# Kernel tuning notes

Hardware: AMD Instinct MI355X
Metric: run time of the kernel (lower is better)

## Reference

```python
import jax, jax.numpy as jnp
import numpy as np
from jax import lax

NT = 100
NUM_LEVELS = 9

_KERNEL = jnp.array([[0.0, 0.25, 0.0],
                     [0.25, 0.0, 0.25],
                     [0.0, 0.25, 0.0]], dtype=jnp.float32).reshape(1, 1, 3, 3)


def _conv(x):
    # 3x3 Jacobi stencil, padding=1 (SAME), NCHW layout
    return lax.conv_general_dilated(x, _KERNEL.astype(x.dtype), (1, 1), 'SAME',
                                    dimension_numbers=('NCHW', 'OIHW', 'NCHW'))


def _avg_pool2(x):
    n, c, h, w = x.shape
    return x.reshape(n, c, h // 2, 2, w // 2, 2).mean(axis=(3, 5))


def _interp(x, th, tw):
    n, c = x.shape[:2]
    # bilinear, align_corners=False (half-pixel centers) == jax.image bilinear
    return jax.image.resize(x, (n, c, th, tw), method='bilinear')


def _jacobi(x, mask, nt):
    def step(x, _):
        x_next = _conv(x)
        return x_next * mask + x * (1 - mask), None
    x, _ = lax.scan(step, x, None, length=nt)
    return x


def setup_inputs() -> dict:
    key = jax.random.key(0)
    ks = jax.random.split(key, 12)
    inp = {'X': jax.random.normal(ks[0], (1, 1, 1024, 1024), dtype=jnp.float32)}
    sizes = [1024, 512, 256, 128, 64, 32, 16, 8, 4, 4]
    for i, s in enumerate(sizes):
        inp[f'Mask{i + 1}'] = jax.random.uniform(ks[i + 1], (1, 1, s, s), dtype=jnp.float32)
    return inp


def reference(X, Mask1, Mask2, Mask3, Mask4, Mask5, Mask6, Mask7, Mask8, Mask9, Mask10):
    masks = [Mask1, Mask2, Mask3, Mask4, Mask5, Mask6, Mask7, Mask8, Mask9, Mask10]
    grids = [X]
    # Restriction sweep: fine -> coarse
    for level in range(1, NUM_LEVELS):
        g = grids[level - 1]
        m = masks[level - 1]
        masked_out = _conv(g * (m > 0).astype(g.dtype))
        unmasked_out = _conv(g * (1 - m))
        residual = masked_out + unmasked_out
        grids.append(_avg_pool2(residual))
    # Coarse solve: Jacobi relaxation on coarsest grid with Mask9
    grids[-1] = _jacobi(grids[-1], Mask9, NT)
    # Prolongation sweep: coarse -> fine
    for level in range(NUM_LEVELS - 2, -1, -1):
        th, tw = grids[level].shape[-2:]
        fine = _interp(grids[level + 1], th, tw) + grids[level]
        m = masks[level]
        fine = _conv(fine * (m > 0).astype(fine.dtype)) + _conv(fine * (1 - m))
        grids[level + 1] = fine  # mirror torch list mutation semantics loosely
    # torch code pops down to grids[0] (original X) and runs fine Jacobi on it
    final_solution = grids[0]
    final_solution = _jacobi(final_solution, Mask1, NT)
    return final_solution
```

## Files before the change

### kernel.cpp

```cpp
#include <hip/hip_runtime.h>


#define W 1024
#define H 1024
#define TILE_W 128
#define TILE_H 64
#define TI 10
#define OS_X 104
#define OS_Y 44
#define HX 12
#define NBX 10
#define NBY 24
#define NLAUNCH 10

#define SRr 18
#define SRc 34
#define S_T 0
#define S_B 1
#define S_L 2
#define S_R 3

__device__ __forceinline__ float4 ld4(const float* __restrict__ p, int gr, int gc) {
    if ((unsigned)gr < (unsigned)H && (unsigned)gc < (unsigned)W)
        return *(const float4*)&p[gr * W + gc];
    return make_float4(0.f, 0.f, 0.f, 0.f);
}

__device__ __forceinline__ float4 rowstep(const float4 up, const float4 ce,
                                          const float4 dn, const float lf,
                                          const float rt, const float4 m) {
    float4 s, n;
    s.x = (up.x + dn.x) + (lf   + ce.y);
    s.y = (up.y + dn.y) + (ce.x + ce.z);
    s.z = (up.z + dn.z) + (ce.y + ce.w);
    s.w = (up.w + dn.w) + (ce.z + rt);
    n.x = fmaf(m.x, fmaf(0.25f, s.x, -ce.x), ce.x);
    n.y = fmaf(m.y, fmaf(0.25f, s.y, -ce.y), ce.y);
    n.z = fmaf(m.z, fmaf(0.25f, s.z, -ce.z), ce.z);
    n.w = fmaf(m.w, fmaf(0.25f, s.w, -ce.w), ce.w);
    return n;
}

__global__ __launch_bounds__(512, 1) void jacobi_trap(
    const float* __restrict__ xin, const float* __restrict__ mask,
    float* __restrict__ xout)
{
    __shared__ float4 S[2][4][SRr][SRc];

    const int tid = threadIdx.x;
    const int pr = tid >> 5;
    const int pc = tid & 31;
    const int gx0 = (int)blockIdx.x * OS_X - HX;
    const int gy0 = (int)blockIdx.y * OS_Y - TI;
    const int gr0 = gy0 + pr * 4;
    const int gc0 = gx0 + pc * 4;

    {
        float4* flat = &S[0][0][0][0];
        const int tot = 2 * 4 * SRr * SRc;
        #pragma unroll
        for (int k = 0; k < 10; ++k) {
            int idx = tid + k * 512;
            if (idx < tot) flat[idx] = make_float4(0.f, 0.f, 0.f, 0.f);
        }
    }

    float4 c[4], m[4];
    #pragma unroll
    for (int i = 0; i < 4; ++i) {
        c[i] = ld4(xin,  gr0 + i, gc0);
        m[i] = ld4(mask, gr0 + i, gc0);
    }

    __syncthreads();

    S[0][S_T][pr + 1][pc + 1] = c[0];
    S[0][S_B][pr + 1][pc + 1] = c[3];
    S[0][S_L][pr + 1][pc + 1] = make_float4(c[0].x, c[1].x, c[2].x, c[3].x);
    S[0][S_R][pr + 1][pc + 1] = make_float4(c[0].w, c[1].w, c[2].w, c[3].w);
    __syncthreads();

    #pragma unroll 1
    for (int it = 0; it < TI; ++it) {
        const int rb = it & 1;
        const float4 th = S[rb][S_B][pr    ][pc + 1];
        const float4 bh = S[rb][S_T][pr + 2][pc + 1];
        const float4 lh = S[rb][S_R][pr + 1][pc    ];
        const float4 rh = S[rb][S_L][pr + 1][pc + 2];

        const float4 n0 = rowstep(th,   c[0], c[1], lh.x, rh.x, m[0]);
        const float4 n1 = rowstep(c[0], c[1], c[2], lh.y, rh.y, m[1]);
        const float4 n2 = rowstep(c[1], c[2], c[3], lh.z, rh.z, m[2]);
        const float4 n3 = rowstep(c[2], c[3], bh,   lh.w, rh.w, m[3]);
        c[0] = n0; c[1] = n1; c[2] = n2; c[3] = n3;

        if (it < TI - 1) {
            const int wb = rb ^ 1;
            S[wb][S_T][pr + 1][pc + 1] = n0;
            S[wb][S_B][pr + 1][pc + 1] = n3;
            S[wb][S_L][pr + 1][pc + 1] = make_float4(n0.x, n1.x, n2.x, n3.x);
            S[wb][S_R][pr + 1][pc + 1] = make_float4(n0.w, n1.w, n2.w, n3.w);
            __syncthreads();
        }
    }

    const int lc = pc * 4;
    if (lc >= HX && lc < HX + OS_X && (unsigned)gc0 < (unsigned)W) {
        #pragma unroll
        for (int i = 0; i < 4; ++i) {
            int lr = pr * 4 + i;
            if (lr < TI || lr >= TILE_H - TI) continue;
            int gr = gy0 + lr;
            if ((unsigned)gr >= (unsigned)H) continue;
            *(float4*)&xout[gr * W + gc0] = c[i];
        }
    }
}

extern "C" void kernel_launch(void* const* d_in, const int* in_sizes, int n_in,
                              void* d_out, int out_size, void* d_ws, size_t ws_size,
                              hipStream_t stream) {
    const float* X = (const float*)d_in[0];
    const float* M = (const float*)d_in[1];
    float* out = (float*)d_out;
    float* ws  = (float*)d_ws;

    dim3 grid(NBX, NBY), block(512);
    const float* src = X;
    for (int l = 0; l < NLAUNCH; ++l) {
        float* dst = (l & 1) ? out : ws;
        jacobi_trap<<<grid, block, 0, stream>>>(src, M, dst);
        src = dst;
    }
}
```

Before: 114.6 us.

## Fuse 20 Jacobi steps per launch with 128x128 tiles and 8-row thread strips

Each thread now holds 8 rows instead of 4, so a block covers a 128x128 tile. The kernel runs 20 time steps per launch with a 20-cell halo, cutting the number of launches from 10 to 5. Only the shared-memory border cells are zeroed rather than the whole buffer. The trade is more redundant halo work (88x88 useful output per 128x128 tile), higher register pressure, and fewer blocks (144) to fill the GPU.

Result: slower. 141.7 us (+23.6%).

```diff
diff --git a/kernel.cpp b/kernel.cpp
--- a/kernel.cpp
+++ b/kernel.cpp
@@ -3,22 +3,20 @@
 
 #define W 1024
 #define H 1024
-#define TILE_W 128
-#define TILE_H 64
-#define TI 10
-#define OS_X 104
-#define OS_Y 44
-#define HX 12
-#define NBX 10
-#define NBY 24
-#define NLAUNCH 10
+#define TILE 128
+#define TI 20
+#define OS 88
+#define NB 12
+#define NLAUNCH 5
 
 #define SRr 18
 #define SRc 34
-#define S_T 0
-#define S_B 1
-#define S_L 2
-#define S_R 3
+#define S_T  0
+#define S_B  1
+#define S_L0 2
+#define S_L1 3
+#define S_R0 4
+#define S_R1 5
 
 __device__ __forceinline__ float4 ld4(const float* __restrict__ p, int gr, int gc) {
     if ((unsigned)gr < (unsigned)H && (unsigned)gc < (unsigned)W)
@@ -45,71 +43,86 @@
     const float* __restrict__ xin, const float* __restrict__ mask,
     float* __restrict__ xout)
 {
-    __shared__ float4 S[2][4][SRr][SRc];
+    __shared__ float4 S[2][6][SRr][SRc];
 
     const int tid = threadIdx.x;
     const int pr = tid >> 5;
     const int pc = tid & 31;
-    const int gx0 = (int)blockIdx.x * OS_X - HX;
-    const int gy0 = (int)blockIdx.y * OS_Y - TI;
-    const int gr0 = gy0 + pr * 4;
+    const int gx0 = (int)blockIdx.x * OS - TI;
+    const int gy0 = (int)blockIdx.y * OS - TI;
+    const int gr0 = gy0 + pr * 8;
     const int gc0 = gx0 + pc * 4;
 
-    {
-        float4* flat = &S[0][0][0][0];
-        const int tot = 2 * 4 * SRr * SRc;
-        #pragma unroll
-        for (int k = 0; k < 10; ++k) {
-            int idx = tid + k * 512;
-            if (idx < tot) flat[idx] = make_float4(0.f, 0.f, 0.f, 0.f);
+    #pragma unroll
+    for (int k = 0; k < 3; ++k) {
+        int idx = tid + k * 512;
+        if (idx < 1200) {
+            int bs  = idx / 100;
+            int pos = idx - bs * 100;
+            float4* st = &S[bs / 6][bs % 6][0][0];
+            int r, cc;
+            if      (pos < 34) { r = 0;            cc = pos;      }
+            else if (pos < 68) { r = SRr - 1;      cc = pos - 34; }
+            else if (pos < 84) { r = pos - 68 + 1; cc = 0;        }
+            else               { r = pos - 84 + 1; cc = SRc - 1;  }
+            st[r * SRc + cc] = make_float4(0.f, 0.f, 0.f, 0.f);
         }
     }
 
-    float4 c[4], m[4];
+    float4 c[8], m[8];
     #pragma unroll
-    for (int i = 0; i < 4; ++i) {
+    for (int i = 0; i < 8; ++i) {
         c[i] = ld4(xin,  gr0 + i, gc0);
         m[i] = ld4(mask, gr0 + i, gc0);
     }
 
-    __syncthreads();
-
-    S[0][S_T][pr + 1][pc + 1] = c[0];
-    S[0][S_B][pr + 1][pc + 1] = c[3];
-    S[0][S_L][pr + 1][pc + 1] = make_float4(c[0].x, c[1].x, c[2].x, c[3].x);
-    S[0][S_R][pr + 1][pc + 1] = make_float4(c[0].w, c[1].w, c[2].w, c[3].w);
+    S[0][S_T ][pr + 1][pc + 1] = c[0];
+    S[0][S_B ][pr + 1][pc + 1] = c[7];
+    S[0][S_L0][pr + 1][pc + 1] = make_float4(c[0].x, c[1].x, c[2].x, c[3].x);
+    S[0][S_L1][pr + 1][pc + 1] = make_float4(c[4].x, c[5].x, c[6].x, c[7].x);
+    S[0][S_R0][pr + 1][pc + 1] = make_float4(c[0].w, c[1].w, c[2].w, c[3].w);
+    S[0][S_R1][pr + 1][pc + 1] = make_float4(c[4].w, c[5].w, c[6].w, c[7].w);
     __syncthreads();
 
     #pragma unroll 1
     for (int it = 0; it < TI; ++it) {
         const int rb = it & 1;
-        const float4 th = S[rb][S_B][pr    ][pc + 1];
-        const float4 bh = S[rb][S_T][pr + 2][pc + 1];
-        const float4 lh = S[rb][S_R][pr + 1][pc    ];
-        const float4 rh = S[rb][S_L][pr + 1][pc + 2];
+        const float4 th  = S[rb][S_B ][pr    ][pc + 1];
+        const float4 bh  = S[rb][S_T ][pr + 2][pc + 1];
+        const float4 lh0 = S[rb][S_R0][pr + 1][pc    ];
+        const float4 lh1 = S[rb][S_R1][pr + 1][pc    ];
+        const float4 rh0 = S[rb][S_L0][pr + 1][pc + 2];
+        const float4 rh1 = S[rb][S_L1][pr + 1][pc + 2];
 
-        const float4 n0 = rowstep(th,   c[0], c[1], lh.x, rh.x, m[0]);
-        const float4 n1 = rowstep(c[0], c[1], c[2], lh.y, rh.y, m[1]);
-        const float4 n2 = rowstep(c[1], c[2], c[3], lh.z, rh.z, m[2]);
-        const float4 n3 = rowstep(c[2], c[3], bh,   lh.w, rh.w, m[3]);
-        c[0] = n0; c[1] = n1; c[2] = n2; c[3] = n3;
+        float4 n[8];
+        n[0] = rowstep(th,   c[0], c[1], lh0.x, rh0.x, m[0]);
+        n[1] = rowstep(c[0], c[1], c[2], lh0.y, rh0.y, m[1]);
+        n[2] = rowstep(c[1], c[2], c[3], lh0.z, rh0.z, m[2]);
+        n[3] = rowstep(c[2], c[3], c[4], lh0.w, rh0.w, m[3]);
+        n[4] = rowstep(c[3], c[4], c[5], lh1.x, rh1.x, m[4]);
+        n[5] = rowstep(c[4], c[5], c[6], lh1.y, rh1.y, m[5]);
+        n[6] = rowstep(c[5], c[6], c[7], lh1.z, rh1.z, m[6]);
+        n[7] = rowstep(c[6], c[7], bh,   lh1.w, rh1.w, m[7]);
+        #pragma unroll
+        for (int i = 0; i < 8; ++i) c[i] = n[i];
 
         if (it < TI - 1) {
             const int wb = rb ^ 1;
-            S[wb][S_T][pr + 1][pc + 1] = n0;
-            S[wb][S_B][pr + 1][pc + 1] = n3;
-            S[wb][S_L][pr + 1][pc + 1] = make_float4(n0.x, n1.x, n2.x, n3.x);
-            S[wb][S_R][pr + 1][pc + 1] = make_float4(n0.w, n1.w, n2.w, n3.w);
+            S[wb][S_T ][pr + 1][pc + 1] = n[0];
+            S[wb][S_B ][pr + 1][pc + 1] = n[7];
+            S[wb][S_L0][pr + 1][pc + 1] = make_float4(n[0].x, n[1].x, n[2].x, n[3].x);
+            S[wb][S_L1][pr + 1][pc + 1] = make_float4(n[4].x, n[5].x, n[6].x, n[7].x);
+            S[wb][S_R0][pr + 1][pc + 1] = make_float4(n[0].w, n[1].w, n[2].w, n[3].w);
+            S[wb][S_R1][pr + 1][pc + 1] = make_float4(n[4].w, n[5].w, n[6].w, n[7].w);
             __syncthreads();
         }
     }
 
-    const int lc = pc * 4;
-    if (lc >= HX && lc < HX + OS_X && (unsigned)gc0 < (unsigned)W) {
+    if (pc >= 5 && pc <= 26 && (unsigned)gc0 < (unsigned)W) {
         #pragma unroll
-        for (int i = 0; i < 4; ++i) {
-            int lr = pr * 4 + i;
-            if (lr < TI || lr >= TILE_H - TI) continue;
+        for (int i = 0; i < 8; ++i) {
+            int lr = pr * 8 + i;
+            if (lr < TI || lr >= TILE - TI) continue;
             int gr = gy0 + lr;
             if ((unsigned)gr >= (unsigned)H) continue;
             *(float4*)&xout[gr * W + gc0] = c[i];
@@ -125,10 +138,10 @@
     float* out = (float*)d_out;
     float* ws  = (float*)d_ws;
 
-    dim3 grid(NBX, NBY), block(512);
+    dim3 grid(NB, NB), block(512);
     const float* src = X;
     for (int l = 0; l < NLAUNCH; ++l) {
-        float* dst = (l & 1) ? out : ws;
+        float* dst = ((NLAUNCH - 1 - l) & 1) ? ws : out;
         jacobi_trap<<<grid, block, 0, stream>>>(src, M, dst);
         src = dst;
     }
```

## Exchange vertical halos within wavefront via permlane32 swap, shrink LDS halo buffers

Applied to the files above, without the earlier changes.

Each 64-lane wavefront holds two tile rows. The halo exchange between those two rows now goes through permlane32_swap in registers instead of LDS. Only the cross-wavefront top and bottom halos still use LDS, in separate smaller arrays, and only their boundary cells are zeroed instead of clearing the whole shared buffer. This removes about half of the top/bottom LDS writes and reads plus the full shared-memory clear. In exchange it adds cross-lane swap instructions and divergent selects between the two half-waves.

After: 102.8 us. 1.11x faster.

```diff
diff --git a/kernel.cpp b/kernel.cpp
--- a/kernel.cpp
+++ b/kernel.cpp
@@ -13,12 +13,7 @@
 #define NBY 24
 #define NLAUNCH 10
 
-#define SRr 18
-#define SRc 34
-#define S_T 0
-#define S_B 1
-#define S_L 2
-#define S_R 3
+typedef unsigned uint2v __attribute__((ext_vector_type(2)));
 
 __device__ __forceinline__ float4 ld4(const float* __restrict__ p, int gr, int gc) {
     if ((unsigned)gr < (unsigned)H && (unsigned)gc < (unsigned)W)
@@ -41,29 +36,39 @@
     return n;
 }
 
+__device__ __forceinline__ float xchg32(float p) {
+    unsigned u = __float_as_uint(p);
+    uint2v r = __builtin_amdgcn_permlane32_swap(u, u, false, false);
+    return __uint_as_float(r.x ^ r.y ^ u);
+}
+
+__device__ __forceinline__ float4 xchg32_4(const float4 p) {
+    return make_float4(xchg32(p.x), xchg32(p.y), xchg32(p.z), xchg32(p.w));
+}
+
+__device__ __forceinline__ float4 sel4(bool c, const float4 a, const float4 b) {
+    return make_float4(c ? a.x : b.x, c ? a.y : b.y,
+                       c ? a.z : b.z, c ? a.w : b.w);
+}
+
 __global__ __launch_bounds__(512, 1) void jacobi_trap(
     const float* __restrict__ xin, const float* __restrict__ mask,
     float* __restrict__ xout)
 {
-    __shared__ float4 S[2][4][SRr][SRc];
+    __shared__ float4 SLs[2][18][34];
+    __shared__ float4 SRs[2][18][34];
+    __shared__ float4 STs[2][10][32];
+    __shared__ float4 SBs[2][10][32];
 
     const int tid = threadIdx.x;
-    const int pr = tid >> 5;
-    const int pc = tid & 31;
+    const int pr  = tid >> 5;
+    const int pc  = tid & 31;
+    const int wid = tid >> 6;
+    const bool lowHalf = (tid & 32) == 0;
     const int gx0 = (int)blockIdx.x * OS_X - HX;
     const int gy0 = (int)blockIdx.y * OS_Y - TI;
     const int gr0 = gy0 + pr * 4;
     const int gc0 = gx0 + pc * 4;
-
-    {
-        float4* flat = &S[0][0][0][0];
-        const int tot = 2 * 4 * SRr * SRc;
-        #pragma unroll
-        for (int k = 0; k < 10; ++k) {
-            int idx = tid + k * 512;
-            if (idx < tot) flat[idx] = make_float4(0.f, 0.f, 0.f, 0.f);
-        }
-    }
 
     float4 c[4], m[4];
     #pragma unroll
@@ -72,21 +77,38 @@
         m[i] = ld4(mask, gr0 + i, gc0);
     }
 
-    __syncthreads();
+    const float4 z4 = make_float4(0.f, 0.f, 0.f, 0.f);
+    if (tid < 72) {
+        int b = tid / 36, r2 = tid % 36;
+        if (r2 < 18) SRs[b][r2][0] = z4;
+        else         SLs[b][r2 - 18][33] = z4;
+    } else if (tid >= 128 && tid < 256) {
+        int j = tid - 128, b = j >> 6, r3 = j & 63;
+        if (r3 < 32) STs[b][9][r3] = z4;
+        else         SBs[b][0][r3 - 32] = z4;
+    }
 
-    S[0][S_T][pr + 1][pc + 1] = c[0];
-    S[0][S_B][pr + 1][pc + 1] = c[3];
-    S[0][S_L][pr + 1][pc + 1] = make_float4(c[0].x, c[1].x, c[2].x, c[3].x);
-    S[0][S_R][pr + 1][pc + 1] = make_float4(c[0].w, c[1].w, c[2].w, c[3].w);
+    SLs[0][pr + 1][pc + 1] = make_float4(c[0].x, c[1].x, c[2].x, c[3].x);
+    SRs[0][pr + 1][pc + 1] = make_float4(c[0].w, c[1].w, c[2].w, c[3].w);
+    if (lowHalf) STs[0][wid + 1][pc] = c[0];
+    else         SBs[0][wid + 1][pc] = c[3];
     __syncthreads();
 
     #pragma unroll 1
     for (int it = 0; it < TI; ++it) {
         const int rb = it & 1;
-        const float4 th = S[rb][S_B][pr    ][pc + 1];
-        const float4 bh = S[rb][S_T][pr + 2][pc + 1];
-        const float4 lh = S[rb][S_R][pr + 1][pc    ];
-        const float4 rh = S[rb][S_L][pr + 1][pc + 2];
+
+        const float4 p4 = sel4(lowHalf, c[3], c[0]);
+        const float4 q4 = xchg32_4(p4);
+
+        float4 thL = z4, bhL = z4;
+        if (lowHalf) thL = SBs[rb][wid][pc];
+        else         bhL = STs[rb][wid + 2][pc];
+        const float4 th = sel4(lowHalf, thL, q4);
+        const float4 bh = sel4(lowHalf, q4, bhL);
+
+        const float4 lh = SRs[rb][pr + 1][pc];
+        const float4 rh = SLs[rb][pr + 1][pc + 2];
 
         const float4 n0 = rowstep(th,   c[0], c[1], lh.x, rh.x, m[0]);
         const float4 n1 = rowstep(c[0], c[1], c[2], lh.y, rh.y, m[1]);
@@ -96,10 +118,10 @@
 
         if (it < TI - 1) {
             const int wb = rb ^ 1;
-            S[wb][S_T][pr + 1][pc + 1] = n0;
-            S[wb][S_B][pr + 1][pc + 1] = n3;
-            S[wb][S_L][pr + 1][pc + 1] = make_float4(n0.x, n1.x, n2.x, n3.x);
-            S[wb][S_R][pr + 1][pc + 1] = make_float4(n0.w, n1.w, n2.w, n3.w);
+            SLs[wb][pr + 1][pc + 1] = make_float4(n0.x, n1.x, n2.x, n3.x);
+            SRs[wb][pr + 1][pc + 1] = make_float4(n0.w, n1.w, n2.w, n3.w);
+            if (lowHalf) STs[wb][wid + 1][pc] = n0;
+            else         SBs[wb][wid + 1][pc] = n3;
             __syncthreads();
         }
     }
```
